# Performance work log

Hardware: AMD Instinct MI355X
Metric: run time of the kernel (lower is better)

Reference implementation:

```python
import jax, jax.numpy as jnp
import numpy as np

B, S, D, H, DK = 2, 2048, 1024, 16, 64  # batch, seq, d_model, heads, head_dim


def setup_inputs() -> dict:
    key = jax.random.key(0)
    ks = jax.random.split(key, 11)
    inp = {
        "v": jax.random.normal(ks[0], (B, S, D), dtype=jnp.float32),
        "k": jax.random.normal(ks[1], (B, S, D), dtype=jnp.float32),
        "q": jax.random.normal(ks[2], (B, S, D), dtype=jnp.float32),
        # per-head Linear(d_model, d_k): torch weight shape [d_k, d_model], stacked over heads
        "Wq": jax.random.normal(ks[3], (H, DK, D), dtype=jnp.float32) * 0.02,
        "bq": jax.random.normal(ks[4], (H, DK), dtype=jnp.float32) * 0.02,
        "Wk": jax.random.normal(ks[5], (H, DK, D), dtype=jnp.float32) * 0.02,
        "bk": jax.random.normal(ks[6], (H, DK), dtype=jnp.float32) * 0.02,
        "Wv": jax.random.normal(ks[7], (H, DK, D), dtype=jnp.float32) * 0.02,
        "bv": jax.random.normal(ks[8], (H, DK), dtype=jnp.float32) * 0.02,
        "Wo": jax.random.normal(ks[9], (D, D), dtype=jnp.float32) * 0.02,
        "bo": jax.random.normal(ks[10], (D,), dtype=jnp.float32) * 0.02,
    }
    return inp


def reference(v, k, q, Wq, bq, Wk, bk, Wv, bv, Wo, bo):
    # Batched per-head projections (original uses a python loop over h Linears).
    # torch Linear: y = x @ W.T + b  ->  einsum over last dim of W.
    q2 = jnp.einsum("bsd,hkd->bhsk", q, Wq) + bq[None, :, None, :]
    k2 = jnp.einsum("bsd,hkd->bhsk", k, Wk) + bk[None, :, None, :]
    v2 = jnp.einsum("bsd,hkd->bhsk", v, Wv) + bv[None, :, None, :]
    # FAITHFUL to source bug: attention(v2, k2, q2) -> scores from v2 @ k2^T,
    # softmax, then weighted sum of q2. (dropout = identity in eval mode)
    scores = jnp.einsum("bhsk,bhtk->bhst", v2, k2) / jnp.sqrt(jnp.float32(DK))
    attn = jax.nn.softmax(scores, axis=-1)
    out = jnp.einsum("bhst,bhtk->bhsk", attn, q2)
    # concat heads in order (head i -> slice [i*d_k:(i+1)*d_k])
    out = out.transpose(0, 2, 1, 3).reshape(B, S, H * DK)
    return out @ Wo.T + bo
```

## Files before the change

### kernel.cpp

```cpp
#include <hip/hip_runtime.h>
#include <stdint.h>

#define B_  2
#define S_  2048
#define D_  1024
#define H_  16
#define DK_ 64
#define VST 2176

typedef unsigned short u16;
typedef short bf16x8 __attribute__((ext_vector_type(8)));
typedef float f32x4  __attribute__((ext_vector_type(4)));

#define MFMA(a,b,c) __builtin_amdgcn_mfma_f32_16x16x32_bf16((a),(b),(c),0,0,0)
#define EXP2(x) __builtin_amdgcn_exp2f(x)

static __device__ __forceinline__ u16 f2bf(float f) {
    uint32_t u = __float_as_uint(f);
    u += 0x7fffu + ((u >> 16) & 1u);
    return (u16)(u >> 16);
}

typedef const __attribute__((address_space(1))) void* gas_p;
typedef __attribute__((address_space(3))) void* las_p;
static __device__ __forceinline__ void gld16(const u16* g, u16* l) {
    __builtin_amdgcn_global_load_lds((gas_p)g, (las_p)l, 16, 0, 0);
}


__global__ void conv3(const float* __restrict__ a, const float* __restrict__ b,
                      const float* __restrict__ c,
                      u16* __restrict__ da, u16* __restrict__ db, u16* __restrict__ dc) {
    const int z = blockIdx.y;
    const float* s = (z == 0) ? a : (z == 1 ? b : c);
    u16* d = (z == 0) ? da : (z == 1 ? db : dc);
    const int i = (blockIdx.x * 256 + threadIdx.x) * 4;
    float4 f = *(const float4*)(s + i);
    ushort4 o;
    o.x = f2bf(f.x); o.y = f2bf(f.y); o.z = f2bf(f.z); o.w = f2bf(f.w);
    *(ushort4*)(d + i) = o;
}

__global__ void conv4(const float* __restrict__ a, const float* __restrict__ b,
                      const float* __restrict__ c, const float* __restrict__ e,
                      u16* __restrict__ da, u16* __restrict__ db,
                      u16* __restrict__ dc, u16* __restrict__ de) {
    const int z = blockIdx.y;
    const float* s = (z == 0) ? a : (z == 1 ? b : (z == 2 ? c : e));
    u16* d = (z == 0) ? da : (z == 1 ? db : (z == 2 ? dc : de));
    const int i = (blockIdx.x * 256 + threadIdx.x) * 4;
    float4 f = *(const float4*)(s + i);
    ushort4 o;
    o.x = f2bf(f.x); o.y = f2bf(f.y); o.z = f2bf(f.z); o.w = f2bf(f.w);
    *(ushort4*)(d + i) = o;
}


__global__ __launch_bounds__(256) void proj_gemm(
    const u16* __restrict__ vb, const u16* __restrict__ kb, const u16* __restrict__ qb,
    const u16* __restrict__ Wvb, const u16* __restrict__ Wkb, const u16* __restrict__ Wqb,
    const float* __restrict__ bv, const float* __restrict__ bk, const float* __restrict__ bq,
    u16* __restrict__ v2, u16* __restrict__ k2, u16* __restrict__ q2T)
{
    __shared__ u16 lA[128 * 32];
    __shared__ u16 lB[128 * 32];

    const int z = blockIdx.z;
    const u16* A = (z == 0) ? vb : (z == 1 ? kb : qb);
    const u16* W = (z == 0) ? Wvb : (z == 1 ? Wkb : Wqb);
    const float* bias = (z == 0) ? bv : (z == 1 ? bk : bq);

    const int tid = threadIdx.x;
    const int lane = tid & 63, wave = tid >> 6;
    const int wm = wave >> 1, wn = wave & 1;
    const int q = lane >> 4, l15 = lane & 15;
    const int q4 = q * 4;

    const int rowbase = blockIdx.y * 128;
    const int colbase = blockIdx.x * 128;

    const int srow = wave * 32 + (lane >> 2);
    const int scol = (lane & 3) * 8;
    const u16* gA = A + (size_t)(rowbase + srow) * D_ + scol;
    const u16* gW = W + (size_t)(colbase + srow) * D_ + scol;
    u16* lAp = &lA[srow * 32 + scol];
    u16* lBp = &lB[srow * 32 + scol];

    const int aoff = (wm * 64 + l15) * 32 + q * 8;
    const int boff = (wn * 64 + l15) * 32 + q * 8;

    f32x4 acc[4][4] = {};

    for (int k0 = 0; k0 < D_; k0 += 32) {
        gld16(gA + k0, lAp);
        gld16(gA + k0 + 16 * D_, lAp + 16 * 32);
        gld16(gW + k0, lBp);
        gld16(gW + k0 + 16 * D_, lBp + 16 * 32);
        __syncthreads();
        bf16x8 af[4], bfr[4];
        #pragma unroll
        for (int mi = 0; mi < 4; mi++)
            af[mi] = *(const bf16x8*)&lA[aoff + mi * 512];
        #pragma unroll
        for (int ni = 0; ni < 4; ni++)
            bfr[ni] = *(const bf16x8*)&lB[boff + ni * 512];
        #pragma unroll
        for (int mi = 0; mi < 4; mi++)
            #pragma unroll
            for (int ni = 0; ni < 4; ni++)
                acc[mi][ni] = MFMA(af[mi], bfr[ni], acc[mi][ni]);
        __syncthreads();
    }

    if (z < 2) {
        u16* outp = (z == 0) ? v2 : k2;
        const float scale = (z == 0) ? 0.18033688011112042f : 1.0f;
        #pragma unroll
        for (int mi = 0; mi < 4; mi++) {
            #pragma unroll
            for (int ni = 0; ni < 4; ni++) {
                const int c = colbase + wn * 64 + ni * 16 + l15;
                const int h = c >> 6, dk = c & 63;
                const float bc = bias[c];
                #pragma unroll
                for (int rg = 0; rg < 4; rg++) {
                    const int r = rowbase + wm * 64 + mi * 16 + q4 + rg;
                    const int bb = r >> 11, s = r & (S_ - 1);
                    outp[(size_t)(((bb * H_ + h) * S_) + s) * DK_ + dk] =
                        f2bf((acc[mi][ni][rg] + bc) * scale);
                }
            }
        }
    } else {
        #pragma unroll
        for (int mi = 0; mi < 4; mi++) {
            const int r0 = rowbase + wm * 64 + mi * 16 + q4;
            const int bb = r0 >> 11, s = r0 & (S_ - 1);
            #pragma unroll
            for (int ni = 0; ni < 4; ni++) {
                const int c = colbase + wn * 64 + ni * 16 + l15;
                const int h = c >> 6, dk = c & 63;
                const float bc = bias[c];
                ushort4 o4;
                o4.x = f2bf(acc[mi][ni][0] + bc);
                o4.y = f2bf(acc[mi][ni][1] + bc);
                o4.z = f2bf(acc[mi][ni][2] + bc);
                o4.w = f2bf(acc[mi][ni][3] + bc);
                *(ushort4*)(q2T + (size_t)((bb * H_ + h) * DK_ + dk) * VST + s) = o4;
            }
        }
    }
}


__global__ __launch_bounds__(256) void flash_attn(
    const u16* __restrict__ v2, const u16* __restrict__ k2,
    const u16* __restrict__ q2T, u16* __restrict__ Ob)
{
    __shared__ alignas(16) u16 lK[2][64 * 64];
    __shared__ alignas(16) u16 lV[2][64 * 64];
    __shared__ alignas(16) u16 ldsP[4][2][16][68];

    const int tid = threadIdx.x;
    const int lane = tid & 63, wave = tid >> 6;
    const int q = lane >> 4, l15 = lane & 15;
    const int q4 = q * 4;
    const int bh = blockIdx.y;
    const int sbase = blockIdx.x * 128;

    const u16* Qp = v2  + (size_t)bh * S_ * DK_;
    const u16* Kp = k2  + (size_t)bh * S_ * DK_;
    const u16* Vp = q2T + (size_t)bh * DK_ * VST;

    const int srow8 = lane >> 3;
    const int cs    = lane & 7;
    const int cg    = cs ^ srow8;
    const int krow0 = wave * 16 + srow8;

    bf16x8 bq[2][2];
    #pragma unroll
    for (int g = 0; g < 2; g++) {
        const u16* qp = Qp + (size_t)(sbase + g * 64 + wave * 16 + l15) * DK_ + q * 8;
        bq[g][0] = *(const bf16x8*)(qp);
        bq[g][1] = *(const bf16x8*)(qp + 32);
    }

    bf16x8 ones;
    #pragma unroll
    for (int i = 0; i < 8; i++) ones[i] = (short)0x3F80;

    f32x4 o_acc[2][4] = {};
    f32x4 o_l[2] = {};

    const int sw = l15 & 7;
    const int fc0 = (q ^ sw) * 8;
    const int fc1 = fc0 ^ 32;

    {
        const u16* kg = Kp + (size_t)krow0 * DK_ + cg * 8;
        const u16* vg = Vp + (size_t)krow0 * VST + cg * 8;
        u16* lkd = &lK[0][(wave * 128) * 8 + lane * 8];
        u16* lvd = &lV[0][(wave * 128) * 8 + lane * 8];
        gld16(kg, lkd);
        gld16(kg + 8 * DK_, lkd + 64 * 8);
        gld16(vg, lvd);
        gld16(vg + (size_t)8 * VST, lvd + 64 * 8);
    }

    for (int it = 0; it < S_ / 64; ++it) {
        const int buf = it & 1;
        __syncthreads();
        if (it + 1 < S_ / 64) {
            const int nb = (it + 1) & 1;
            const int t1 = (it + 1) * 64;
            const u16* kg = Kp + (size_t)(t1 + krow0) * DK_ + cg * 8;
            const u16* vg = Vp + (size_t)krow0 * VST + t1 + cg * 8;
            u16* lkd = &lK[nb][(wave * 128) * 8 + lane * 8];
            u16* lvd = &lV[nb][(wave * 128) * 8 + lane * 8];
            gld16(kg, lkd);
            gld16(kg + 8 * DK_, lkd + 64 * 8);
            gld16(vg, lvd);
            gld16(vg + (size_t)8 * VST, lvd + 64 * 8);
        }

        f32x4 s_acc[2][4];
        #pragma unroll
        for (int mi = 0; mi < 4; mi++) {
            const int trow = mi * 16 + l15;
            bf16x8 a0 = *(const bf16x8*)&lK[buf][trow * 64 + fc0];
            bf16x8 a1 = *(const bf16x8*)&lK[buf][trow * 64 + fc1];
            #pragma unroll
            for (int g = 0; g < 2; g++) {
                f32x4 zz = {};
                zz = MFMA(a0, bq[g][0], zz);
                s_acc[g][mi] = MFMA(a1, bq[g][1], zz);
            }
        }

        #pragma unroll
        for (int g = 0; g < 2; g++)
            #pragma unroll
            for (int mi = 0; mi < 4; mi++) {
                float p0 = EXP2(s_acc[g][mi][0]);
                float p1 = EXP2(s_acc[g][mi][1]);
                float p2 = EXP2(s_acc[g][mi][2]);
                float p3 = EXP2(s_acc[g][mi][3]);
                uint2 pk;
                pk.x = __builtin_amdgcn_perm(__float_as_uint(p1), __float_as_uint(p0), 0x07060302u);
                pk.y = __builtin_amdgcn_perm(__float_as_uint(p3), __float_as_uint(p2), 0x07060302u);
                *(uint2*)&ldsP[wave][g][l15][mi * 16 + q4] = pk;
            }

        asm volatile("s_waitcnt lgkmcnt(0)" ::: "memory");

        bf16x8 bp[2][2];
        #pragma unroll
        for (int g = 0; g < 2; g++) {
            uint2* r0 = (uint2*)&bp[g][0];
            r0[0] = *(const uint2*)&ldsP[wave][g][l15][q * 8];
            r0[1] = *(const uint2*)&ldsP[wave][g][l15][q * 8 + 4];
            uint2* r1 = (uint2*)&bp[g][1];
            r1[0] = *(const uint2*)&ldsP[wave][g][l15][32 + q * 8];
            r1[1] = *(const uint2*)&ldsP[wave][g][l15][32 + q * 8 + 4];
        }

        #pragma unroll
        for (int mi = 0; mi < 4; mi++) {
            const int dkrow = mi * 16 + l15;
            bf16x8 av0 = *(const bf16x8*)&lV[buf][dkrow * 64 + fc0];
            bf16x8 av1 = *(const bf16x8*)&lV[buf][dkrow * 64 + fc1];
            #pragma unroll
            for (int g = 0; g < 2; g++) {
                o_acc[g][mi] = MFMA(av0, bp[g][0], o_acc[g][mi]);
                o_acc[g][mi] = MFMA(av1, bp[g][1], o_acc[g][mi]);
            }
        }
        #pragma unroll
        for (int g = 0; g < 2; g++) {
            o_l[g] = MFMA(ones, bp[g][0], o_l[g]);
            o_l[g] = MFMA(ones, bp[g][1], o_l[g]);
        }

        asm volatile("s_barrier" ::: "memory");
    }

    const int bb = bh >> 4, h = bh & 15;
    #pragma unroll
    for (int g = 0; g < 2; g++) {
        const float inv_l = 1.0f / o_l[g][0];
        const int s = sbase + g * 64 + wave * 16 + l15;
        #pragma unroll
        for (int mi = 0; mi < 4; mi++) {
            ushort4 o4;
            o4.x = f2bf(o_acc[g][mi][0] * inv_l);
            o4.y = f2bf(o_acc[g][mi][1] * inv_l);
            o4.z = f2bf(o_acc[g][mi][2] * inv_l);
            o4.w = f2bf(o_acc[g][mi][3] * inv_l);
            *(ushort4*)(Ob + (size_t)(bb * S_ + s) * (H_ * DK_) + h * DK_ + mi * 16 + q4) = o4;
        }
    }
}


__global__ __launch_bounds__(256) void out_gemm(
    const u16* __restrict__ Ob, const u16* __restrict__ Wob,
    const float* __restrict__ bo, float* __restrict__ out)
{
    __shared__ u16 lA[128 * 32];
    __shared__ u16 lB[64 * 32];

    const int tid = threadIdx.x;
    const int lane = tid & 63, wave = tid >> 6;
    const int wm = wave >> 1, wn = wave & 1;
    const int q = lane >> 4, l15 = lane & 15;
    const int q4 = q * 4;

    const int rowbase = blockIdx.y * 128;
    const int colbase = blockIdx.x * 64;

    const int arow = wave * 32 + (lane >> 2);
    const int brow = wave * 16 + (lane >> 2);
    const int scol = (lane & 3) * 8;
    const u16* gA = Ob  + (size_t)(rowbase + arow) * D_ + scol;
    const u16* gW = Wob + (size_t)(colbase + brow) * D_ + scol;
    u16* lAp = &lA[arow * 32 + scol];
    u16* lBp = &lB[brow * 32 + scol];

    const int aoff = (wm * 64 + l15) * 32 + q * 8;
    const int boff = (wn * 32 + l15) * 32 + q * 8;

    f32x4 acc[4][2] = {};

    for (int k0 = 0; k0 < D_; k0 += 32) {
        gld16(gA + k0, lAp);
        gld16(gA + k0 + 16 * D_, lAp + 16 * 32);
        gld16(gW + k0, lBp);
        __syncthreads();
        bf16x8 af[4], bfr[2];
        #pragma unroll
        for (int mi = 0; mi < 4; mi++)
            af[mi] = *(const bf16x8*)&lA[aoff + mi * 512];
        #pragma unroll
        for (int ni = 0; ni < 2; ni++)
            bfr[ni] = *(const bf16x8*)&lB[boff + ni * 512];
        #pragma unroll
        for (int mi = 0; mi < 4; mi++)
            #pragma unroll
            for (int ni = 0; ni < 2; ni++)
                acc[mi][ni] = MFMA(af[mi], bfr[ni], acc[mi][ni]);
        __syncthreads();
    }

    #pragma unroll
    for (int mi = 0; mi < 4; mi++)
        #pragma unroll
        for (int ni = 0; ni < 2; ni++) {
            const int c = colbase + wn * 32 + ni * 16 + l15;
            const float bc = bo[c];
            #pragma unroll
            for (int rg = 0; rg < 4; rg++) {
                const int r = rowbase + wm * 64 + mi * 16 + q4 + rg;
                out[(size_t)r * D_ + c] = acc[mi][ni][rg] + bc;
            }
        }
}


extern "C" void kernel_launch(void* const* d_in, const int* in_sizes, int n_in,
                              void* d_out, int out_size, void* d_ws, size_t ws_size,
                              hipStream_t stream) {
    const float* v  = (const float*)d_in[0];
    const float* k  = (const float*)d_in[1];
    const float* qq = (const float*)d_in[2];
    const float* Wq = (const float*)d_in[3];
    const float* bq = (const float*)d_in[4];
    const float* Wk = (const float*)d_in[5];
    const float* bk = (const float*)d_in[6];
    const float* Wv = (const float*)d_in[7];
    const float* bv = (const float*)d_in[8];
    const float* Wo = (const float*)d_in[9];
    const float* bo = (const float*)d_in[10];
    float* out = (float*)d_out;

    char* w = (char*)d_ws;
    u16* vb  = (u16*)(w + 0);
    u16* Ob  = (u16*)(w + 0);
    u16* kb  = (u16*)(w + 8388608);
    u16* qb  = (u16*)(w + 16777216);
    u16* Wqb = (u16*)(w + 25165824);
    u16* Wkb = (u16*)(w + 27262976);
    u16* Wvb = (u16*)(w + 29360128);
    u16* Wob = (u16*)(w + 31457280);
    u16* v2  = (u16*)(w + 33554432);
    u16* k2  = (u16*)(w + 41943040);
    u16* q2T = (u16*)(w + 50331648);

    conv3<<<dim3(4096, 3), 256, 0, stream>>>(v, k, qq, vb, kb, qb);
    conv4<<<dim3(1024, 4), 256, 0, stream>>>(Wq, Wk, Wv, Wo, Wqb, Wkb, Wvb, Wob);
    proj_gemm<<<dim3(8, 32, 3), 256, 0, stream>>>(vb, kb, qb, Wvb, Wkb, Wqb,
                                                  bv, bk, bq, v2, k2, q2T);
    flash_attn<<<dim3(16, 32), 256, 0, stream>>>(v2, k2, q2T, Ob);
    out_gemm<<<dim3(16, 32), 256, 0, stream>>>(Ob, Wob, bo, out);
}
```

Baseline: 248.2 us.

## Fuse fp32-to-bf16 conversion into GEMM loads and stage epilogue stores through LDS

Drops the separate conv3/conv4 conversion kernels. The projection and output GEMMs now load fp32 activations and weights directly into swizzled LDS and convert to bf16 in registers before each MFMA. The projection epilogue writes through an LDS staging buffer so global stores become contiguous 16-byte rows. Block indices are remapped in all three kernels so neighbouring blocks share rows, which should improve L2 locality. In exchange, the GEMMs move twice as many bytes per tile from global memory and pay for conversion on every tile reuse.

```diff
diff --git a/kernel.cpp b/kernel.cpp
--- a/kernel.cpp
+++ b/kernel.cpp
@@ -20,54 +20,38 @@
     u += 0x7fffu + ((u >> 16) & 1u);
     return (u16)(u >> 16);
 }
+static __device__ __forceinline__ uint32_t pk2(float x, float y) {
+    return __builtin_amdgcn_perm(__float_as_uint(y) + 0x8000u,
+                                 __float_as_uint(x) + 0x8000u, 0x07060302u);
+}
+static __device__ __forceinline__ bf16x8 cvt8(float4 a, float4 b) {
+    union { uint32_t u[4]; bf16x8 v; } r;
+    r.u[0] = pk2(a.x, a.y); r.u[1] = pk2(a.z, a.w);
+    r.u[2] = pk2(b.x, b.y); r.u[3] = pk2(b.z, b.w);
+    return r.v;
+}
 
 typedef const __attribute__((address_space(1))) void* gas_p;
 typedef __attribute__((address_space(3))) void* las_p;
-static __device__ __forceinline__ void gld16(const u16* g, u16* l) {
+static __device__ __forceinline__ void gld16(const void* g, void* l) {
     __builtin_amdgcn_global_load_lds((gas_p)g, (las_p)l, 16, 0, 0);
 }
 
 
-__global__ void conv3(const float* __restrict__ a, const float* __restrict__ b,
-                      const float* __restrict__ c,
-                      u16* __restrict__ da, u16* __restrict__ db, u16* __restrict__ dc) {
-    const int z = blockIdx.y;
-    const float* s = (z == 0) ? a : (z == 1 ? b : c);
-    u16* d = (z == 0) ? da : (z == 1 ? db : dc);
-    const int i = (blockIdx.x * 256 + threadIdx.x) * 4;
-    float4 f = *(const float4*)(s + i);
-    ushort4 o;
-    o.x = f2bf(f.x); o.y = f2bf(f.y); o.z = f2bf(f.z); o.w = f2bf(f.w);
-    *(ushort4*)(d + i) = o;
-}
-
-__global__ void conv4(const float* __restrict__ a, const float* __restrict__ b,
-                      const float* __restrict__ c, const float* __restrict__ e,
-                      u16* __restrict__ da, u16* __restrict__ db,
-                      u16* __restrict__ dc, u16* __restrict__ de) {
-    const int z = blockIdx.y;
-    const float* s = (z == 0) ? a : (z == 1 ? b : (z == 2 ? c : e));
-    u16* d = (z == 0) ? da : (z == 1 ? db : (z == 2 ? dc : de));
-    const int i = (blockIdx.x * 256 + threadIdx.x) * 4;
-    float4 f = *(const float4*)(s + i);
-    ushort4 o;
-    o.x = f2bf(f.x); o.y = f2bf(f.y); o.z = f2bf(f.z); o.w = f2bf(f.w);
-    *(ushort4*)(d + i) = o;
-}
-
-
 __global__ __launch_bounds__(256) void proj_gemm(
-    const u16* __restrict__ vb, const u16* __restrict__ kb, const u16* __restrict__ qb,
-    const u16* __restrict__ Wvb, const u16* __restrict__ Wkb, const u16* __restrict__ Wqb,
+    const float* __restrict__ Xv, const float* __restrict__ Xk, const float* __restrict__ Xq,
+    const float* __restrict__ Wv, const float* __restrict__ Wk, const float* __restrict__ Wq,
     const float* __restrict__ bv, const float* __restrict__ bk, const float* __restrict__ bq,
     u16* __restrict__ v2, u16* __restrict__ k2, u16* __restrict__ q2T)
 {
-    __shared__ u16 lA[128 * 32];
-    __shared__ u16 lB[128 * 32];
+    __shared__ alignas(16) char smem[40960];
+    float* lA = (float*)smem;
+    float* lB = (float*)(smem + 16384);
+    u16*   epi = (u16*)smem;
 
     const int z = blockIdx.z;
-    const u16* A = (z == 0) ? vb : (z == 1 ? kb : qb);
-    const u16* W = (z == 0) ? Wvb : (z == 1 ? Wkb : Wqb);
+    const float* A = (z == 0) ? Xv : (z == 1 ? Xk : Xq);
+    const float* W = (z == 0) ? Wv : (z == 1 ? Wk : Wq);
     const float* bias = (z == 0) ? bv : (z == 1 ? bk : bq);
 
     const int tid = threadIdx.x;
@@ -76,34 +60,43 @@
     const int q = lane >> 4, l15 = lane & 15;
     const int q4 = q * 4;
 
-    const int rowbase = blockIdx.y * 128;
-    const int colbase = blockIdx.x * 128;
-
-    const int srow = wave * 32 + (lane >> 2);
-    const int scol = (lane & 3) * 8;
-    const u16* gA = A + (size_t)(rowbase + srow) * D_ + scol;
-    const u16* gW = W + (size_t)(colbase + srow) * D_ + scol;
-    u16* lAp = &lA[srow * 32 + scol];
-    u16* lBp = &lB[srow * 32 + scol];
-
-    const int aoff = (wm * 64 + l15) * 32 + q * 8;
-    const int boff = (wn * 64 + l15) * 32 + q * 8;
+    const int f = blockIdx.y * 8 + blockIdx.x;
+    const int rowbase = (f & 31) * 128;
+    const int colbase = (f >> 5) * 128;
+
+    const int srow8 = lane >> 3;
+    const int cs = lane & 7;
+    const int cg = cs ^ srow8;
+    const float* gA = A + (size_t)(rowbase + wave * 32 + srow8) * D_ + cg * 4;
+    const float* gW = W + (size_t)(colbase + wave * 32 + srow8) * D_ + cg * 4;
+    float* lAp = lA + (wave * 32 + srow8) * 32 + cs * 4;
+    float* lBp = lB + (wave * 32 + srow8) * 32 + cs * 4;
+
+    const int sw = l15 & 7;
+    const int ca = ((2 * q) ^ sw) * 4;
+    const int cb = ((2 * q + 1) ^ sw) * 4;
 
     f32x4 acc[4][4] = {};
 
     for (int k0 = 0; k0 < D_; k0 += 32) {
-        gld16(gA + k0, lAp);
-        gld16(gA + k0 + 16 * D_, lAp + 16 * 32);
-        gld16(gW + k0, lBp);
-        gld16(gW + k0 + 16 * D_, lBp + 16 * 32);
+        #pragma unroll
+        for (int j = 0; j < 4; j++)
+            gld16(gA + k0 + j * 8 * D_, lAp + j * 8 * 32);
+        #pragma unroll
+        for (int j = 0; j < 4; j++)
+            gld16(gW + k0 + j * 8 * D_, lBp + j * 8 * 32);
         __syncthreads();
         bf16x8 af[4], bfr[4];
         #pragma unroll
-        for (int mi = 0; mi < 4; mi++)
-            af[mi] = *(const bf16x8*)&lA[aoff + mi * 512];
-        #pragma unroll
-        for (int ni = 0; ni < 4; ni++)
-            bfr[ni] = *(const bf16x8*)&lB[boff + ni * 512];
+        for (int mi = 0; mi < 4; mi++) {
+            const int r = (wm * 64 + mi * 16 + l15) * 32;
+            af[mi] = cvt8(*(const float4*)&lA[r + ca], *(const float4*)&lA[r + cb]);
+        }
+        #pragma unroll
+        for (int ni = 0; ni < 4; ni++) {
+            const int r = (wn * 64 + ni * 16 + l15) * 32;
+            bfr[ni] = cvt8(*(const float4*)&lB[r + ca], *(const float4*)&lB[r + cb]);
+        }
         #pragma unroll
         for (int mi = 0; mi < 4; mi++)
             #pragma unroll
@@ -112,43 +105,47 @@
         __syncthreads();
     }
 
+    u16* ep = epi + wave * (64 * 80);
+    const int h = (colbase + wn * 64) >> 6;
+    const int Mrow0 = rowbase + wm * 64;
+    const int bb = Mrow0 >> 11;
+
     if (z < 2) {
         u16* outp = (z == 0) ? v2 : k2;
         const float scale = (z == 0) ? 0.18033688011112042f : 1.0f;
         #pragma unroll
-        for (int mi = 0; mi < 4; mi++) {
+        for (int mi = 0; mi < 4; mi++)
             #pragma unroll
             for (int ni = 0; ni < 4; ni++) {
-                const int c = colbase + wn * 64 + ni * 16 + l15;
-                const int h = c >> 6, dk = c & 63;
-                const float bc = bias[c];
+                const float bc = bias[colbase + wn * 64 + ni * 16 + l15];
                 #pragma unroll
-                for (int rg = 0; rg < 4; rg++) {
-                    const int r = rowbase + wm * 64 + mi * 16 + q4 + rg;
-                    const int bb = r >> 11, s = r & (S_ - 1);
-                    outp[(size_t)(((bb * H_ + h) * S_) + s) * DK_ + dk] =
+                for (int rg = 0; rg < 4; rg++)
+                    ep[(mi * 16 + q4 + rg) * 80 + ni * 16 + l15] =
                         f2bf((acc[mi][ni][rg] + bc) * scale);
-                }
-            }
-        }
+            }
+        asm volatile("s_waitcnt lgkmcnt(0)" ::: "memory");
+        const int s = (Mrow0 + lane) & (S_ - 1);
+        u16* gb = outp + ((size_t)(bb * H_ + h) * S_ + s) * DK_;
+        #pragma unroll
+        for (int j = 0; j < 8; j++)
+            *(uint4*)(gb + j * 8) = *(const uint4*)&ep[lane * 80 + j * 8];
     } else {
         #pragma unroll
-        for (int mi = 0; mi < 4; mi++) {
-            const int r0 = rowbase + wm * 64 + mi * 16 + q4;
-            const int bb = r0 >> 11, s = r0 & (S_ - 1);
+        for (int mi = 0; mi < 4; mi++)
             #pragma unroll
             for (int ni = 0; ni < 4; ni++) {
-                const int c = colbase + wn * 64 + ni * 16 + l15;
-                const int h = c >> 6, dk = c & 63;
-                const float bc = bias[c];
-                ushort4 o4;
-                o4.x = f2bf(acc[mi][ni][0] + bc);
-                o4.y = f2bf(acc[mi][ni][1] + bc);
-                o4.z = f2bf(acc[mi][ni][2] + bc);
-                o4.w = f2bf(acc[mi][ni][3] + bc);
-                *(ushort4*)(q2T + (size_t)((bb * H_ + h) * DK_ + dk) * VST + s) = o4;
-            }
-        }
+                const float bc = bias[colbase + wn * 64 + ni * 16 + l15];
+                uint2 pk;
+                pk.x = pk2(acc[mi][ni][0] + bc, acc[mi][ni][1] + bc);
+                pk.y = pk2(acc[mi][ni][2] + bc, acc[mi][ni][3] + bc);
+                *(uint2*)&ep[(ni * 16 + l15) * 80 + mi * 16 + q4] = pk;
+            }
+        asm volatile("s_waitcnt lgkmcnt(0)" ::: "memory");
+        const int s0g = Mrow0 & (S_ - 1);
+        u16* gb = q2T + ((size_t)(bb * H_ + h) * DK_ + lane) * VST + s0g;
+        #pragma unroll
+        for (int j = 0; j < 8; j++)
+            *(uint4*)(gb + j * 8) = *(const uint4*)&ep[lane * 80 + j * 8];
     }
 }
 
@@ -165,8 +162,8 @@
     const int lane = tid & 63, wave = tid >> 6;
     const int q = lane >> 4, l15 = lane & 15;
     const int q4 = q * 4;
-    const int bh = blockIdx.y;
-    const int sbase = blockIdx.x * 128;
+    const int bh = blockIdx.x & 31;
+    const int sbase = (blockIdx.x >> 5) * 128;
 
     const u16* Qp = v2  + (size_t)bh * S_ * DK_;
     const u16* Kp = k2  + (size_t)bh * S_ * DK_;
@@ -303,11 +300,11 @@
 
 
 __global__ __launch_bounds__(256) void out_gemm(
-    const u16* __restrict__ Ob, const u16* __restrict__ Wob,
+    const u16* __restrict__ Ob, const float* __restrict__ Wo,
     const float* __restrict__ bo, float* __restrict__ out)
 {
-    __shared__ u16 lA[128 * 32];
-    __shared__ u16 lB[64 * 32];
+    __shared__ alignas(16) u16 lA[128 * 32];
+    __shared__ alignas(16) float lB[64 * 32];
 
     const int tid = threadIdx.x;
     const int lane = tid & 63, wave = tid >> 6;
@@ -315,19 +312,25 @@
     const int q = lane >> 4, l15 = lane & 15;
     const int q4 = q * 4;
 
-    const int rowbase = blockIdx.y * 128;
-    const int colbase = blockIdx.x * 64;
+    const int f = blockIdx.y * 16 + blockIdx.x;
+    const int rowbase = (f & 31) * 128;
+    const int colbase = (f >> 5) * 64;
 
     const int arow = wave * 32 + (lane >> 2);
-    const int brow = wave * 16 + (lane >> 2);
-    const int scol = (lane & 3) * 8;
-    const u16* gA = Ob  + (size_t)(rowbase + arow) * D_ + scol;
-    const u16* gW = Wob + (size_t)(colbase + brow) * D_ + scol;
-    u16* lAp = &lA[arow * 32 + scol];
-    u16* lBp = &lB[brow * 32 + scol];
+    const int ascol = (lane & 3) * 8;
+    const u16* gA = Ob + (size_t)(rowbase + arow) * D_ + ascol;
+    u16* lAp = &lA[arow * 32 + ascol];
+
+    const int srow8 = lane >> 3;
+    const int cs = lane & 7;
+    const int cg = cs ^ srow8;
+    const float* gW = Wo + (size_t)(colbase + wave * 16 + srow8) * D_ + cg * 4;
+    float* lBp = lB + (wave * 16 + srow8) * 32 + cs * 4;
 
     const int aoff = (wm * 64 + l15) * 32 + q * 8;
-    const int boff = (wn * 32 + l15) * 32 + q * 8;
+    const int sw = l15 & 7;
+    const int ca = ((2 * q) ^ sw) * 4;
+    const int cb = ((2 * q + 1) ^ sw) * 4;
 
     f32x4 acc[4][2] = {};
 
@@ -335,14 +338,17 @@
         gld16(gA + k0, lAp);
         gld16(gA + k0 + 16 * D_, lAp + 16 * 32);
         gld16(gW + k0, lBp);
+        gld16(gW + k0 + 8 * D_, lBp + 8 * 32);
         __syncthreads();
         bf16x8 af[4], bfr[2];
         #pragma unroll
         for (int mi = 0; mi < 4; mi++)
             af[mi] = *(const bf16x8*)&lA[aoff + mi * 512];
         #pragma unroll
-        for (int ni = 0; ni < 2; ni++)
-            bfr[ni] = *(const bf16x8*)&lB[boff + ni * 512];
+        for (int ni = 0; ni < 2; ni++) {
+            const int r = (wn * 32 + ni * 16 + l15) * 32;
+            bfr[ni] = cvt8(*(const float4*)&lB[r + ca], *(const float4*)&lB[r + cb]);
+        }
         #pragma unroll
         for (int mi = 0; mi < 4; mi++)
             #pragma unroll
@@ -383,22 +389,13 @@
     float* out = (float*)d_out;
 
     char* w = (char*)d_ws;
-    u16* vb  = (u16*)(w + 0);
-    u16* Ob  = (u16*)(w + 0);
-    u16* kb  = (u16*)(w + 8388608);
-    u16* qb  = (u16*)(w + 16777216);
-    u16* Wqb = (u16*)(w + 25165824);
-    u16* Wkb = (u16*)(w + 27262976);
-    u16* Wvb = (u16*)(w + 29360128);
-    u16* Wob = (u16*)(w + 31457280);
-    u16* v2  = (u16*)(w + 33554432);
-    u16* k2  = (u16*)(w + 41943040);
-    u16* q2T = (u16*)(w + 50331648);
-
-    conv3<<<dim3(4096, 3), 256, 0, stream>>>(v, k, qq, vb, kb, qb);
-    conv4<<<dim3(1024, 4), 256, 0, stream>>>(Wq, Wk, Wv, Wo, Wqb, Wkb, Wvb, Wob);
-    proj_gemm<<<dim3(8, 32, 3), 256, 0, stream>>>(vb, kb, qb, Wvb, Wkb, Wqb,
+    u16* v2  = (u16*)(w + 0);
+    u16* k2  = (u16*)(w + 8388608);
+    u16* q2T = (u16*)(w + 16777216);
+    u16* Ob  = (u16*)(w + 25690112);
+
+    proj_gemm<<<dim3(8, 32, 3), 256, 0, stream>>>(v, k, qq, Wv, Wk, Wq,
                                                   bv, bk, bq, v2, k2, q2T);
-    flash_attn<<<dim3(16, 32), 256, 0, stream>>>(v2, k2, q2T, Ob);
-    out_gemm<<<dim3(16, 32), 256, 0, stream>>>(Ob, Wob, bo, out);
-}
+    flash_attn<<<dim3(512), 256, 0, stream>>>(v2, k2, q2T, Ob);
+    out_gemm<<<dim3(16, 32), 256, 0, stream>>>(Ob, Wo, bo, out);
+}
```

New measurement: 278.3 us. +12.1%, slower.
